# Kernel tuning notes

Hardware: AMD Instinct MI355X
Metric: run time of the kernel (lower is better)

The kernel has to match this reference:

```python
import jax, jax.numpy as jnp
import numpy as np

# Steady-state MemoryBank contrastive loss (post-warmup, all banks full).
B, D = 1024, 128            # batch, feature_dim
C, K = 50, 4096             # num_classes, per-class bank capacity (memory_size // num_classes)
TEMP = 0.3
TAIL_CLASSES = (0, 1)
TAIL_WEIGHT = 1.3
EPS = 1e-12                 # F.normalize eps


def setup_inputs() -> dict:
    key = jax.random.key(0)
    k1, k2, k3 = jax.random.split(key, 3)
    features = jax.random.normal(k1, (B, D), dtype=jnp.float32)
    labels = jax.random.randint(k2, (B,), 0, C)
    # memory_bank_c buffers, stacked: [C, K, D] (registered as randn in __init__)
    memory = jax.random.normal(k3, (C, K, D), dtype=jnp.float32)
    return {"features": features, "labels": labels, "memory": memory}


def reference(features, labels, memory):
    # L2-normalize features (F.normalize with eps clamp)
    norm = jnp.maximum(jnp.linalg.norm(features, axis=1, keepdims=True), EPS)
    feat = features / norm                                   # [B, D]

    # Similarities of every sample to every bank row, scaled by temperature.
    sims = jnp.einsum('bd,ckd->bck', feat, memory) / TEMP    # [B, C, K]

    # Cross-entropy with target index 0 over concat([pos_bank, neg_banks]):
    # target logit is the first row of the positive (label) bank; the
    # normalizer is logsumexp over ALL bank rows (order-invariant).
    pos_logit = sims[jnp.arange(B), labels, 0]               # [B]
    lse = jax.nn.logsumexp(sims.reshape(B, C * K), axis=1)   # [B]
    per_sample = lse - pos_logit                             # -log softmax[0]

    tail = jnp.isin(labels, jnp.asarray(TAIL_CLASSES))
    weights = jnp.where(tail, TAIL_WEIGHT, 1.0)
    # All B samples are valid in steady state -> divide by B.
    return jnp.sum(weights * per_sample) / B
```

## Files before the change

### kernel.cpp

```cpp
#include <hip/hip_runtime.h>


#define XCHUNK 128
#define NITER 25
#define TILE_BYTES 32768
#define LN2f 0.6931471805599453f
#define SCALEf 4.808983469629878f

typedef __attribute__((ext_vector_type(8))) short bf16x8;
typedef __attribute__((ext_vector_type(4))) float f32x4;
typedef unsigned int u32;

__device__ __forceinline__ unsigned short f2bf(float x) {
    union { float f; unsigned int u; } c; c.f = x;
    unsigned int u = c.u;
    u = (u + 0x7fffu + ((u >> 16) & 1u)) >> 16;
    return (unsigned short)u;
}
__device__ __forceinline__ float bf2f(unsigned short h) {
    union { unsigned int u; float f; } c; c.u = ((unsigned int)h) << 16;
    return c.f;
}
__device__ __forceinline__ unsigned int pack_bf2(float lo, float hi) {
    union { float f; unsigned int u; } a, b; a.f = lo; b.f = hi;
    return __builtin_amdgcn_perm(b.u, a.u, 0x07060302u);
}

__global__ void normalize_feat(const float* __restrict__ f,
                               unsigned short* __restrict__ featb,
                               float* __restrict__ S,
                               float* __restrict__ out) {
    const int b = blockIdx.x;
    const int t = threadIdx.x;
    if (t == 0) S[b] = 0.0f;
    if (b == 0 && t == 1) *out = 0.0f;
    float v = f[b * 128 + t];
    float ss = v * v;
    #pragma unroll
    for (int m = 1; m < 64; m <<= 1) ss += __shfl_xor(ss, m, 64);
    __shared__ float wsum[2];
    if ((t & 63) == 0) wsum[t >> 6] = ss;
    __syncthreads();
    float tot = wsum[0] + wsum[1];
    float inv = SCALEf / fmaxf(sqrtf(tot), 1e-12f);
    featb[b * 128 + t] = f2bf(v * inv);
}

__global__ __launch_bounds__(512, 4) void gemm_lse(
        const unsigned short* __restrict__ featb,
        const float* __restrict__ mem,
        float* __restrict__ S)
{
    __shared__ uint4 ldsb[2][1024];

    const int tid  = threadIdx.x;
    const int wave = tid >> 6;
    const int lane = tid & 63;
    const int col  = lane & 15;
    const int quad = lane >> 4;

    const int m_wave = blockIdx.y * 256 + wave * 32;
    const int xc = blockIdx.x;

    bf16x8 afrag[2][4];
    #pragma unroll
    for (int mf = 0; mf < 2; ++mf)
        #pragma unroll
        for (int ks = 0; ks < 4; ++ks)
            afrag[mf][ks] = *(const bf16x8*)&featb[(size_t)(m_wave + mf * 16 + col) * 128
                                                   + ks * 32 + quad * 8];

    float s_part[8];
    #pragma unroll
    for (int i = 0; i < 8; ++i) s_part[i] = 0.0f;

    int o[2];
    #pragma unroll
    for (int j = 0; j < 2; ++j) {
        int Sl = j * 512 + tid;
        int Fi = Sl >> 6, L = Sl & 63;
        int snf = Fi >> 2, sks = Fi & 3, sq = L >> 4, sc = L & 15;
        o[j] = (snf * 16 + sc) * 512 + sks * 128 + sq * 32;
    }

    float4 g0a, g0b, g1a, g1b;

    #define LOADS(t_) {                                                         \
        const char* gt = (const char*)mem + (size_t)(xc + XCHUNK * (t_)) * TILE_BYTES; \
        g0a = *(const float4*)(gt + o[0]);                                      \
        g0b = *(const float4*)(gt + o[0] + 16);                                 \
        g1a = *(const float4*)(gt + o[1]);                                      \
        g1b = *(const float4*)(gt + o[1] + 16); }

    #define PACKWRITE(bi) {                                                     \
        uint4 pk;                                                               \
        pk.x = pack_bf2(g0a.x, g0a.y); pk.y = pack_bf2(g0a.z, g0a.w);           \
        pk.z = pack_bf2(g0b.x, g0b.y); pk.w = pack_bf2(g0b.z, g0b.w);           \
        ldsb[bi][tid] = pk;                                                     \
        pk.x = pack_bf2(g1a.x, g1a.y); pk.y = pack_bf2(g1a.z, g1a.w);           \
        pk.z = pack_bf2(g1b.x, g1b.y); pk.w = pack_bf2(g1b.z, g1b.w);           \
        ldsb[bi][512 + tid] = pk; }

    #define COMPUTE(bi) {                                                       \
        _Pragma("unroll")                                                       \
        for (int nf = 0; nf < 4; ++nf) {                                        \
            f32x4 acc[2];                                                       \
            _Pragma("unroll")                                                   \
            for (int mf = 0; mf < 2; ++mf) acc[mf] = (f32x4)(0.0f);             \
            _Pragma("unroll")                                                   \
            for (int ks = 0; ks < 4; ++ks) {                                    \
                bf16x8 bfrag = *(const bf16x8*)&ldsb[bi][(nf * 4 + ks) * 64 + lane]; \
                _Pragma("unroll")                                               \
                for (int mf = 0; mf < 2; ++mf)                                  \
                    acc[mf] = __builtin_amdgcn_mfma_f32_16x16x32_bf16(          \
                        afrag[mf][ks], bfrag, acc[mf], 0, 0, 0);                \
            }                                                                   \
            _Pragma("unroll")                                                   \
            for (int mf = 0; mf < 2; ++mf)                                      \
                _Pragma("unroll")                                               \
                for (int r = 0; r < 4; ++r)                                     \
                    s_part[mf * 4 + r] += __builtin_amdgcn_exp2f(acc[mf][r]);   \
        } }

    LOADS(0)
    PACKWRITE(0)
    __syncthreads();

    for (int t = 0; t < NITER; ++t) {
        if (t + 1 < NITER) LOADS(t + 1)
        COMPUTE(t & 1)
        if (t + 1 < NITER) PACKWRITE((t + 1) & 1)
        __syncthreads();
    }

    #pragma unroll
    for (int d = 1; d < 16; d <<= 1)
        #pragma unroll
        for (int i = 0; i < 8; ++i)
            s_part[i] += __shfl_xor(s_part[i], d, 64);

    if (col == 0) {
        #pragma unroll
        for (int i = 0; i < 8; ++i) {
            int row = m_wave + (i >> 2) * 16 + quad * 4 + (i & 3);
            atomicAdd(&S[row], s_part[i]);
        }
    }
    #undef LOADS
    #undef PACKWRITE
    #undef COMPUTE
}

__global__ void finalize_k(const unsigned short* __restrict__ featb,
                           const float* __restrict__ mem,
                           const int* __restrict__ labels,
                           const float* __restrict__ S,
                           float* __restrict__ out) {
    const int wave = threadIdx.x >> 6;
    const int lane = threadIdx.x & 63;
    const int b = blockIdx.x * 4 + wave;
    const int lab = labels[b];
    const float* mrow = mem + (size_t)lab * (4096 * 128);
    float fa = bf2f(featb[b * 128 + lane]);
    float fc = bf2f(featb[b * 128 + lane + 64]);
    float p = fa * mrow[lane] + fc * mrow[lane + 64];
    #pragma unroll
    for (int m = 1; m < 64; m <<= 1) p += __shfl_xor(p, m, 64);
    if (lane == 0) {
        float w = (lab < 2) ? 1.3f : 1.0f;
        float v = w * LN2f * (log2f(S[b]) - p) * (1.0f / 1024.0f);
        atomicAdd(out, v);
    }
}

extern "C" void kernel_launch(void* const* d_in, const int* in_sizes, int n_in,
                              void* d_out, int out_size, void* d_ws, size_t ws_size,
                              hipStream_t stream) {
    const float* features = (const float*)d_in[0];
    const int*   labels   = (const int*)d_in[1];
    const float* memory   = (const float*)d_in[2];
    float* out = (float*)d_out;

    unsigned short* featb = (unsigned short*)d_ws;
    float* S = (float*)((char*)d_ws + 1024 * 128 * 2);

    normalize_feat<<<1024, 128, 0, stream>>>(features, featb, S, out);
    gemm_lse<<<dim3(XCHUNK, 4), 512, 0, stream>>>(featb, memory, S);
    finalize_k<<<256, 256, 0, stream>>>(featb, memory, labels, S, out);
}
```

Before: 207.4 us.

## Fuse normalization, GEMM-LSE and finalize into one kernel with last-block reduction

```diff
diff --git a/kernel.cpp b/kernel.cpp
--- a/kernel.cpp
+++ b/kernel.cpp
@@ -26,32 +26,20 @@
     return __builtin_amdgcn_perm(b.u, a.u, 0x07060302u);
 }
 
-__global__ void normalize_feat(const float* __restrict__ f,
-                               unsigned short* __restrict__ featb,
-                               float* __restrict__ S,
-                               float* __restrict__ out) {
-    const int b = blockIdx.x;
-    const int t = threadIdx.x;
-    if (t == 0) S[b] = 0.0f;
-    if (b == 0 && t == 1) *out = 0.0f;
-    float v = f[b * 128 + t];
-    float ss = v * v;
-    #pragma unroll
-    for (int m = 1; m < 64; m <<= 1) ss += __shfl_xor(ss, m, 64);
-    __shared__ float wsum[2];
-    if ((t & 63) == 0) wsum[t >> 6] = ss;
-    __syncthreads();
-    float tot = wsum[0] + wsum[1];
-    float inv = SCALEf / fmaxf(sqrtf(tot), 1e-12f);
-    featb[b * 128 + t] = f2bf(v * inv);
-}
-
-__global__ __launch_bounds__(512, 4) void gemm_lse(
-        const unsigned short* __restrict__ featb,
+__global__ __launch_bounds__(512, 4) void fused_loss(
+        const float* __restrict__ features,
+        const int*   __restrict__ labels,
         const float* __restrict__ mem,
-        float* __restrict__ S)
+        float* __restrict__ S,
+        int*   __restrict__ cnt,
+        int*   __restrict__ gcnt,
+        float* __restrict__ finacc,
+        float* __restrict__ out)
 {
     __shared__ uint4 ldsb[2][1024];
+    __shared__ float norms_inv[256];
+    __shared__ float fsum[8];
+    __shared__ int   isLast;
 
     const int tid  = threadIdx.x;
     const int wave = tid >> 6;
@@ -59,16 +47,41 @@
     const int col  = lane & 15;
     const int quad = lane >> 4;
 
-    const int m_wave = blockIdx.y * 256 + wave * 32;
-    const int xc = blockIdx.x;
+    const int y        = blockIdx.y;
+    const int base_row = y * 256;
+    const int xc       = blockIdx.x;
+
+    {
+        int lr = tid >> 1, h = tid & 1;
+        const float4* fr = (const float4*)features + (size_t)(base_row + lr) * 32 + h * 16;
+        float ss = 0.0f;
+        #pragma unroll
+        for (int j = 0; j < 16; ++j) {
+            float4 v = fr[j];
+            ss += v.x * v.x + v.y * v.y + v.z * v.z + v.w * v.w;
+        }
+        ss += __shfl_xor(ss, 1, 64);
+        if (h == 0) norms_inv[lr] = SCALEf / fmaxf(sqrtf(ss), 1e-12f);
+    }
+    __syncthreads();
 
     bf16x8 afrag[2][4];
     #pragma unroll
     for (int mf = 0; mf < 2; ++mf)
         #pragma unroll
-        for (int ks = 0; ks < 4; ++ks)
-            afrag[mf][ks] = *(const bf16x8*)&featb[(size_t)(m_wave + mf * 16 + col) * 128
-                                                   + ks * 32 + quad * 8];
+        for (int ks = 0; ks < 4; ++ks) {
+            int lrow = wave * 32 + mf * 16 + col;
+            const float* fp = features + (size_t)(base_row + lrow) * 128 + ks * 32 + quad * 8;
+            float4 a = *(const float4*)fp;
+            float4 b = *(const float4*)(fp + 4);
+            float inv = norms_inv[lrow];
+            bf16x8 f;
+            f[0] = (short)f2bf(a.x * inv); f[1] = (short)f2bf(a.y * inv);
+            f[2] = (short)f2bf(a.z * inv); f[3] = (short)f2bf(a.w * inv);
+            f[4] = (short)f2bf(b.x * inv); f[5] = (short)f2bf(b.y * inv);
+            f[6] = (short)f2bf(b.z * inv); f[7] = (short)f2bf(b.w * inv);
+            afrag[mf][ks] = f;
+        }
 
     float s_part[8];
     #pragma unroll
@@ -142,35 +155,56 @@
     if (col == 0) {
         #pragma unroll
         for (int i = 0; i < 8; ++i) {
-            int row = m_wave + (i >> 2) * 16 + quad * 4 + (i & 3);
+            int row = base_row + wave * 32 + (i >> 2) * 16 + quad * 4 + (i & 3);
             atomicAdd(&S[row], s_part[i]);
+        }
+    }
+
+    __threadfence();
+    if (tid == 0) {
+        int old = atomicAdd(&cnt[y], 1);
+        isLast = (old == 127);
+    }
+    __syncthreads();
+
+    if (isLast) {
+        float acc = 0.0f;
+        #pragma unroll 2
+        for (int r = 0; r < 32; ++r) {
+            int lr  = wave * 32 + r;
+            int b   = base_row + lr;
+            int lab = labels[b];
+            const float* mrow = mem + (size_t)lab * (4096 * 128);
+            float inv = norms_inv[lr];
+            float fa = bf2f(f2bf(features[(size_t)b * 128 + lane] * inv));
+            float fc = bf2f(f2bf(features[(size_t)b * 128 + lane + 64] * inv));
+            float p = fa * mrow[lane] + fc * mrow[lane + 64];
+            #pragma unroll
+            for (int m = 1; m < 64; m <<= 1) p += __shfl_xor(p, m, 64);
+            if (lane == 0) {
+                float Sb = atomicAdd(&S[b], 0.0f);
+                float w  = (lab < 2) ? 1.3f : 1.0f;
+                acc += w * (log2f(Sb) - p);
+            }
+        }
+        if (lane == 0) fsum[wave] = acc * LN2f;
+        __syncthreads();
+        if (tid == 0) {
+            float tot = 0.0f;
+            #pragma unroll
+            for (int i = 0; i < 8; ++i) tot += fsum[i];
+            atomicAdd(finacc, tot);
+            __threadfence();
+            int o2 = atomicAdd(gcnt, 1);
+            if (o2 == 3) {
+                float v = atomicAdd(finacc, 0.0f);
+                *out = v * (1.0f / 1024.0f);
+            }
         }
     }
     #undef LOADS
     #undef PACKWRITE
     #undef COMPUTE
-}
-
-__global__ void finalize_k(const unsigned short* __restrict__ featb,
-                           const float* __restrict__ mem,
-                           const int* __restrict__ labels,
-                           const float* __restrict__ S,
-                           float* __restrict__ out) {
-    const int wave = threadIdx.x >> 6;
-    const int lane = threadIdx.x & 63;
-    const int b = blockIdx.x * 4 + wave;
-    const int lab = labels[b];
-    const float* mrow = mem + (size_t)lab * (4096 * 128);
-    float fa = bf2f(featb[b * 128 + lane]);
-    float fc = bf2f(featb[b * 128 + lane + 64]);
-    float p = fa * mrow[lane] + fc * mrow[lane + 64];
-    #pragma unroll
-    for (int m = 1; m < 64; m <<= 1) p += __shfl_xor(p, m, 64);
-    if (lane == 0) {
-        float w = (lab < 2) ? 1.3f : 1.0f;
-        float v = w * LN2f * (log2f(S[b]) - p) * (1.0f / 1024.0f);
-        atomicAdd(out, v);
-    }
 }
 
 extern "C" void kernel_launch(void* const* d_in, const int* in_sizes, int n_in,
@@ -181,10 +215,12 @@
     const float* memory   = (const float*)d_in[2];
     float* out = (float*)d_out;
 
-    unsigned short* featb = (unsigned short*)d_ws;
-    float* S = (float*)((char*)d_ws + 1024 * 128 * 2);
-
-    normalize_feat<<<1024, 128, 0, stream>>>(features, featb, S, out);
-    gemm_lse<<<dim3(XCHUNK, 4), 512, 0, stream>>>(featb, memory, S);
-    finalize_k<<<256, 256, 0, stream>>>(featb, memory, labels, S, out);
-}
+    float* S      = (float*)d_ws;
+    int*   cnt    = (int*)((char*)d_ws + 4096);
+    int*   gcnt   = cnt + 4;
+    float* finacc = (float*)(cnt + 6);
+
+    hipMemsetAsync(d_ws, 0, 4096 + 64, stream);
+    fused_loss<<<dim3(XCHUNK, 4), 512, 0, stream>>>(
+        features, labels, memory, S, cnt, gcnt, finacc, out);
+}
```

New measurement: 293.8 us. 1.42x slower.
